# Kernel tuning notes

Measured on AMD Instinct MI355X. Metric: run time of the kernel, lower is better.

## Reference

```python
import jax, jax.numpy as jnp
import numpy as np

N, D, C, G, NNZ = 256, 1024, 50000, 4, 300000
EPS = 1e-5


def setup_inputs() -> dict:
    key = jax.random.key(0)
    ks = jax.random.split(key, 5)
    return {
        "output": jax.random.normal(ks[0], (N, D), jnp.float32),
        "wt2_w": jax.random.normal(ks[1], (C, D), jnp.float32) * 0.02,
        "wt2_b": jnp.zeros((C,), jnp.float32),
        "A_vals": jax.random.uniform(ks[2], (G, NNZ), dtype=jnp.float32),
        "vec": jnp.ones((G,), jnp.float32),
        "A_rows": jax.random.randint(ks[3], (G, NNZ), 0, C, jnp.int32),
        "A_cols": jax.random.randint(ks[4], (G, NNZ), 0, C, jnp.int32),
    }


def reference(output, wt2_w, wt2_b, A_vals, vec, A_rows, A_cols):
    # BatchNorm1d(embed_dim, affine=False), training-mode batch stats (biased var)
    mean = jnp.mean(output, axis=0)
    var = jnp.var(output, axis=0)
    h0 = (output - mean) * jax.lax.rsqrt(var + EPS)
    # wt2 linear + swish -> Z [N, C]
    h1 = h0 @ wt2_w.T + wt2_b
    Z = h1 * jax.nn.sigmoid(h1)
    # multi-graph sparse propagation: neighbors += spmm(A_i * vec[i], Z^T)^T
    # spmm out[b, r] = sum_{e: rows[e]==r} vals[e] * Z[b, cols[e]]
    Zt = Z.T  # [C, N]
    neighbors = jnp.zeros_like(Z)
    n_graphs = A_vals.shape[0]
    for i in range(n_graphs):  # small fixed number of relation graphs
        vals = A_vals[i] * vec[i]               # learnable per-graph weight
        msgs = Zt[A_cols[i]] * vals[:, None]    # [nnz, N] gathered messages
        agg = jax.ops.segment_sum(msgs, A_rows[i], num_segments=Zt.shape[0])  # [C, N]
        neighbors = neighbors + agg.T
    # residual combine
    return neighbors + Z
```

## Files before the change

kernel.cpp:

```cpp
#include <hip/hip_runtime.h>

typedef __attribute__((ext_vector_type(8))) short short8;
typedef __attribute__((ext_vector_type(4))) float floatx4;

#define C_DIM 50000
#define D_DIM 1024
#define N_DIM 256
#define G_NUM 4
#define NNZ_G 300000
#define E_TOT (G_NUM * NNZ_G)
#define SLOT_CAP 64

#define O_SB   0u
#define O_H0   8192u
#define O_ZT   532480u
#define O_CNT  26132480u
#define O_OFF  26332544u
#define O_CUR  26532608u
#define O_BS   26732672u
#define O_EDG  26733696u
#define O_CNT2 26132480u
#define O_SLOT 26332544u
#define SLOT_WS_NEEDED 51932544u

static __device__ __forceinline__ unsigned short f2bf(float f) {
    union { float f; unsigned u; } v; v.f = f;
    unsigned r = v.u + 0x7fffu + ((v.u >> 16) & 1u);
    return (unsigned short)(r >> 16);
}
static __device__ __forceinline__ float bf2f(unsigned short u) {
    union { unsigned u; float f; } v; v.u = ((unsigned)u) << 16;
    return v.f;
}

__global__ __launch_bounds__(256) void k_bnstats(const float* __restrict__ x,
                                                 float* __restrict__ scale,
                                                 float* __restrict__ bias) {
    __shared__ float sms[8][32], smss[8][32];
    const int t = threadIdx.x;
    const int dc = t & 31, grp = t >> 5;
    const int d = blockIdx.x * 32 + dc;
    float s = 0.f, ss = 0.f;
    for (int n = grp; n < N_DIM; n += 8) {
        float v = x[n * D_DIM + d];
        s += v; ss += v * v;
    }
    sms[grp][dc] = s; smss[grp][dc] = ss;
    __syncthreads();
    if (t < 32) {
        float S = 0.f, SS = 0.f;
#pragma unroll
        for (int g2 = 0; g2 < 8; ++g2) { S += sms[g2][t]; SS += smss[g2][t]; }
        float mean = S * (1.f / N_DIM);
        float var  = SS * (1.f / N_DIM) - mean * mean;
        float sc = rsqrtf(var + 1e-5f);
        int dd = blockIdx.x * 32 + t;
        scale[dd] = sc;
        bias[dd] = -mean * sc;
    }
}

__global__ __launch_bounds__(256) void k_h0f(const float* __restrict__ x,
                                             const float* __restrict__ scale,
                                             const float* __restrict__ bias,
                                             unsigned short* __restrict__ h0F) {
    int id = blockIdx.x * 256 + threadIdx.x;
    int b = id >> 7, kc = id & 127;
    const float4* xp = (const float4*)&x[(size_t)b * D_DIM + kc * 8];
    float4 f0 = xp[0], f1 = xp[1];
    const float4* sp = (const float4*)&scale[kc * 8];
    const float4* bp = (const float4*)&bias[kc * 8];
    float4 s0 = sp[0], s1 = sp[1], b0 = bp[0], b1 = bp[1];
    short8 o;
    o[0] = (short)f2bf(f0.x * s0.x + b0.x);
    o[1] = (short)f2bf(f0.y * s0.y + b0.y);
    o[2] = (short)f2bf(f0.z * s0.z + b0.z);
    o[3] = (short)f2bf(f0.w * s0.w + b0.w);
    o[4] = (short)f2bf(f1.x * s1.x + b1.x);
    o[5] = (short)f2bf(f1.y * s1.y + b1.y);
    o[6] = (short)f2bf(f1.z * s1.z + b1.z);
    o[7] = (short)f2bf(f1.w * s1.w + b1.w);
    int off = (b >> 4) * 16384 + (kc >> 2) * 512 + (kc & 3) * 128 + (b & 15) * 8;
    *(short8*)&h0F[off] = o;
}

__global__ __launch_bounds__(256) void k_gemm(const float* __restrict__ W,
                                              const float* __restrict__ wb,
                                              const unsigned short* __restrict__ h0F,
                                              unsigned short* __restrict__ Zt) {
    __shared__ unsigned short A_lds[2][8 * 64 * 8];
    const int t = threadIdx.x;
    const int w = t >> 6, lane = t & 63;
    const int m = lane & 15, g = lane >> 4;
    const int c0 = blockIdx.x * 64;

    const int srow = t >> 4;
    const int scc  = t & 15;
    const int s_kh = scc >> 3;
    const int s_g  = (scc >> 1) & 3;
    const int s_half = scc & 1;
    const int sbase = (srow + 16 * s_g) * 8 + s_half * 4;

    const unsigned short* hb = h0F + (size_t)(w * 4) * 16384 + lane * 8;

    float4 raA[4], raB[4];
    floatx4 acc[4][4];
#pragma unroll
    for (int i = 0; i < 4; ++i)
#pragma unroll
        for (int j = 0; j < 4; ++j) acc[i][j] = (floatx4)0.f;

#define LOADA(RA, ksv)                                                           \
    {                                                                            \
        const int kkv = (ksv) * 64;                                              \
        _Pragma("unroll")                                                        \
        for (int q = 0; q < 4; ++q) {                                            \
            int rr_ = c0 + q * 16 + srow; if (rr_ >= C_DIM) rr_ = C_DIM - 1;     \
            RA[q] = *(const float4*)&W[(size_t)rr_ * D_DIM + kkv + scc * 4];     \
        }                                                                        \
    }
#define STOREA(RA, bufv)                                                          \
    {                                                                             \
        _Pragma("unroll")                                                         \
        for (int q = 0; q < 4; ++q) {                                             \
            float4 f_ = RA[q];                                                    \
            unsigned p0_ = (unsigned)f2bf(f_.x) | ((unsigned)f2bf(f_.y) << 16);   \
            unsigned p1_ = (unsigned)f2bf(f_.z) | ((unsigned)f2bf(f_.w) << 16);   \
            *(uint2*)&A_lds[bufv][(s_kh * 4 + q) * 512 + sbase] =                 \
                make_uint2(p0_, p1_);                                             \
        }                                                                         \
    }
#define BARRIER()                                               \
    asm volatile("s_waitcnt lgkmcnt(0)" ::: "memory");          \
    __builtin_amdgcn_sched_barrier(0);                          \
    __builtin_amdgcn_s_barrier();                               \
    __builtin_amdgcn_sched_barrier(0);

#define GSTEP(ksv, RAs, RAl, CUR)                                                 \
    {                                                                             \
        short8 bfrag[2][4];                                                       \
        _Pragma("unroll")                                                         \
        for (int kh = 0; kh < 2; ++kh)                                            \
            _Pragma("unroll")                                                     \
            for (int j = 0; j < 4; ++j)                                           \
                bfrag[kh][j] = *(const short8*)&hb[(size_t)j * 16384 +            \
                                                  ((ksv) * 2 + kh) * 512];        \
        short8 afrag[2][4];                                                       \
        _Pragma("unroll")                                                         \
        for (int kh = 0; kh < 2; ++kh)                                            \
            _Pragma("unroll")                                                     \
            for (int i = 0; i < 4; ++i)                                           \
                afrag[kh][i] = *(const short8*)&A_lds[CUR][(kh * 4 + i) * 512 +   \
                                                          lane * 8];              \
        if ((ksv) < 15) STOREA(RAs, (CUR) ^ 1)                                    \
        if ((ksv) < 14) LOADA(RAl, (ksv) + 2)                                     \
        __builtin_amdgcn_s_setprio(1);                                            \
        _Pragma("unroll")                                                         \
        for (int kh = 0; kh < 2; ++kh)                                            \
            _Pragma("unroll")                                                     \
            for (int i = 0; i < 4; ++i)                                           \
                _Pragma("unroll")                                                 \
                for (int j = 0; j < 4; ++j)                                       \
                    acc[i][j] = __builtin_amdgcn_mfma_f32_16x16x32_bf16(          \
                        afrag[kh][i], bfrag[kh][j], acc[i][j], 0, 0, 0);          \
        __builtin_amdgcn_s_setprio(0);                                            \
        BARRIER()                                                                 \
    }

    LOADA(raA, 0)
    STOREA(raA, 0)
    LOADA(raB, 1)
    BARRIER()

#pragma unroll 1
    for (int ks2 = 0; ks2 < 16; ks2 += 2) {
        GSTEP(ks2,     raB, raA, 0)
        GSTEP(ks2 + 1, raA, raB, 1)
    }
#undef GSTEP
#undef LOADA
#undef STOREA
#undef BARRIER

#pragma unroll
    for (int i = 0; i < 4; ++i) {
#pragma unroll
        for (int j = 0; j < 4; ++j) {
            int b = w * 64 + j * 16 + m;
#pragma unroll
            for (int rr = 0; rr < 4; ++rr) {
                int c = c0 + i * 16 + g * 4 + rr;
                if (c < C_DIM) {
                    float x = acc[i][j][rr] + wb[c];
                    float z = x / (1.f + __expf(-x));
                    Zt[(size_t)c * 256 + b] = f2bf(z);
                }
            }
        }
    }
}

__global__ __launch_bounds__(256) void k_fscatter(const int* __restrict__ rows,
                                                  const int* __restrict__ cols,
                                                  const float* __restrict__ vals,
                                                  const float* __restrict__ vec,
                                                  int* __restrict__ cnt,
                                                  int2* __restrict__ slot) {
    int id = blockIdx.x * 256 + threadIdx.x;
    if (id < E_TOT) {
        int gidx = id / NNZ_G;
        float v = vals[id] * vec[gidx];
        int r = rows[id];
        int c = cols[id];
        int pos = atomicAdd(&cnt[r], 1);
        if (pos < SLOT_CAP) slot[r * SLOT_CAP + pos] = make_int2(c, __float_as_int(v));
    }
}

__global__ __launch_bounds__(256) void k_count(const int* __restrict__ rows,
                                               int* __restrict__ counts) {
    int id = blockIdx.x * 256 + threadIdx.x;
    if (id < E_TOT) atomicAdd(&counts[rows[id]], 1);
}

__global__ __launch_bounds__(256) void k_scan1(const int* __restrict__ counts,
                                               int* __restrict__ offsets,
                                               int* __restrict__ bsums) {
    __shared__ int sm[256];
    int t = threadIdx.x, i = blockIdx.x * 256 + t;
    int v = (i < C_DIM) ? counts[i] : 0;
    sm[t] = v; __syncthreads();
    for (int off = 1; off < 256; off <<= 1) {
        int x = (t >= off) ? sm[t - off] : 0;
        __syncthreads();
        sm[t] += x;
        __syncthreads();
    }
    if (i < C_DIM) offsets[i] = sm[t] - v;
    if (t == 255) bsums[blockIdx.x] = sm[255];
}

__global__ __launch_bounds__(256) void k_scan2(int* __restrict__ bsums,
                                               int* __restrict__ offsets) {
    __shared__ int sm[256];
    int t = threadIdx.x;
    int v = (t < 196) ? bsums[t] : 0;
    sm[t] = v; __syncthreads();
    for (int off = 1; off < 256; off <<= 1) {
        int x = (t >= off) ? sm[t - off] : 0;
        __syncthreads();
        sm[t] += x;
        __syncthreads();
    }
    if (t < 196) bsums[t] = sm[t] - v;
    if (t == 0) offsets[C_DIM] = sm[255];
}

__global__ __launch_bounds__(256) void k_scan3(const int* __restrict__ bsums,
                                               int* __restrict__ offsets,
                                               int* __restrict__ cursor) {
    int i = blockIdx.x * 256 + threadIdx.x;
    if (i < C_DIM) {
        int off = offsets[i] + bsums[blockIdx.x];
        offsets[i] = off;
        cursor[i] = off;
    }
}

__global__ __launch_bounds__(256) void k_scatter(const int* __restrict__ rows,
                                                 const int* __restrict__ cols,
                                                 const float* __restrict__ vals,
                                                 const float* __restrict__ vec,
                                                 int* __restrict__ cursor,
                                                 int2* __restrict__ edges) {
    int id = blockIdx.x * 256 + threadIdx.x;
    if (id < E_TOT) {
        int gidx = id / NNZ_G;
        float v = vals[id] * vec[gidx];
        int r = rows[id];
        int c = cols[id];
        int pos = atomicAdd(&cursor[r], 1);
        edges[pos] = make_int2(c, __float_as_int(v));
    }
}

static __device__ __forceinline__ void agg_row(const unsigned short* __restrict__ Zt,
                                               const int2* __restrict__ E,
                                               int s, int e, int base,
                                               float& a0, float& a1,
                                               float& a2, float& a3) {
    for (; s + 8 <= e; s += 8) {
        int2 e0 = E[s],     e1 = E[s + 1], e2 = E[s + 2], e3 = E[s + 3];
        int2 e4 = E[s + 4], e5 = E[s + 5], e6 = E[s + 6], e7 = E[s + 7];
        ushort4 g0 = *(const ushort4*)&Zt[(size_t)(unsigned)e0.x * 256 + base];
        ushort4 g1 = *(const ushort4*)&Zt[(size_t)(unsigned)e1.x * 256 + base];
        ushort4 g2 = *(const ushort4*)&Zt[(size_t)(unsigned)e2.x * 256 + base];
        ushort4 g3 = *(const ushort4*)&Zt[(size_t)(unsigned)e3.x * 256 + base];
        ushort4 g4 = *(const ushort4*)&Zt[(size_t)(unsigned)e4.x * 256 + base];
        ushort4 g5 = *(const ushort4*)&Zt[(size_t)(unsigned)e5.x * 256 + base];
        ushort4 g6 = *(const ushort4*)&Zt[(size_t)(unsigned)e6.x * 256 + base];
        ushort4 g7 = *(const ushort4*)&Zt[(size_t)(unsigned)e7.x * 256 + base];
        float v0 = __int_as_float(e0.y), v1 = __int_as_float(e1.y);
        float v2 = __int_as_float(e2.y), v3 = __int_as_float(e3.y);
        float v4 = __int_as_float(e4.y), v5 = __int_as_float(e5.y);
        float v6 = __int_as_float(e6.y), v7 = __int_as_float(e7.y);
        a0 += v0 * bf2f(g0.x) + v1 * bf2f(g1.x) + v2 * bf2f(g2.x) + v3 * bf2f(g3.x)
            + v4 * bf2f(g4.x) + v5 * bf2f(g5.x) + v6 * bf2f(g6.x) + v7 * bf2f(g7.x);
        a1 += v0 * bf2f(g0.y) + v1 * bf2f(g1.y) + v2 * bf2f(g2.y) + v3 * bf2f(g3.y)
            + v4 * bf2f(g4.y) + v5 * bf2f(g5.y) + v6 * bf2f(g6.y) + v7 * bf2f(g7.y);
        a2 += v0 * bf2f(g0.z) + v1 * bf2f(g1.z) + v2 * bf2f(g2.z) + v3 * bf2f(g3.z)
            + v4 * bf2f(g4.z) + v5 * bf2f(g5.z) + v6 * bf2f(g6.z) + v7 * bf2f(g7.z);
        a3 += v0 * bf2f(g0.w) + v1 * bf2f(g1.w) + v2 * bf2f(g2.w) + v3 * bf2f(g3.w)
            + v4 * bf2f(g4.w) + v5 * bf2f(g5.w) + v6 * bf2f(g6.w) + v7 * bf2f(g7.w);
    }
    for (; s < e; ++s) {
        int2 e0 = E[s];
        ushort4 g0 = *(const ushort4*)&Zt[(size_t)(unsigned)e0.x * 256 + base];
        float v0 = __int_as_float(e0.y);
        a0 += v0 * bf2f(g0.x);
        a1 += v0 * bf2f(g0.y);
        a2 += v0 * bf2f(g0.z);
        a3 += v0 * bf2f(g0.w);
    }
}

#define AGG_BODY(SBEG, SEND, EPTR)                                                \
    __shared__ float sm[32 * 256];                                                \
    const int t = threadIdx.x;                                                    \
    const int w = t >> 6, lane = t & 63;                                          \
    const int r0 = blockIdx.x * 32;                                               \
    const int base = lane * 4;                                                    \
    _Pragma("unroll 1")                                                           \
    for (int k = 0; k < 8; ++k) {                                                 \
        int lrow = w * 8 + k;                                                     \
        int r = __builtin_amdgcn_readfirstlane(r0 + lrow);                        \
        if (r < C_DIM) {                                                          \
            ushort4 z = *(const ushort4*)&Zt[(size_t)r * 256 + base];             \
            float a0 = bf2f(z.x), a1 = bf2f(z.y), a2 = bf2f(z.z), a3 = bf2f(z.w); \
            agg_row(Zt, (EPTR), (SBEG), (SEND), base, a0, a1, a2, a3);            \
            *(float4*)&sm[lrow * 256 + base] = make_float4(a0, a1, a2, a3);       \
        }                                                                         \
    }                                                                             \
    __syncthreads();                                                              \
    int rows_ = C_DIM - r0; if (rows_ > 32) rows_ = 32;                           \
    int nq = rows_ >> 2;                                                          \
    float4* op = (float4*)&out[(size_t)t * C_DIM + r0];                           \
    _Pragma("unroll 1")                                                           \
    for (int q = 0; q < nq; ++q) {                                                \
        float4 o;                                                                 \
        o.x = sm[(q * 4 + 0) * 256 + t];                                          \
        o.y = sm[(q * 4 + 1) * 256 + t];                                          \
        o.z = sm[(q * 4 + 2) * 256 + t];                                          \
        o.w = sm[(q * 4 + 3) * 256 + t];                                          \
        op[q] = o;                                                                \
    }

__global__ __launch_bounds__(256) void k_agg_csr(const unsigned short* __restrict__ Zt,
                                                 const int* __restrict__ offsets,
                                                 const int2* __restrict__ edges,
                                                 float* __restrict__ out) {
    AGG_BODY(offsets[r], offsets[r + 1], edges)
}

__global__ __launch_bounds__(256) void k_agg_slot(const unsigned short* __restrict__ Zt,
                                                  const int* __restrict__ cnt,
                                                  const int2* __restrict__ slot,
                                                  float* __restrict__ out) {
    AGG_BODY(r * SLOT_CAP, r * SLOT_CAP + min(cnt[r], SLOT_CAP), slot)
}
#undef AGG_BODY

extern "C" void kernel_launch(void* const* d_in, const int* in_sizes, int n_in,
                              void* d_out, int out_size, void* d_ws, size_t ws_size,
                              hipStream_t stream) {
    (void)in_sizes; (void)n_in; (void)out_size;
    const float* x     = (const float*)d_in[0];
    const float* W     = (const float*)d_in[1];
    const float* wb    = (const float*)d_in[2];
    const float* Avals = (const float*)d_in[3];
    const float* vec   = (const float*)d_in[4];
    const int*   Arows = (const int*)d_in[5];
    const int*   Acols = (const int*)d_in[6];
    float* out = (float*)d_out;
    char* ws = (char*)d_ws;

    float* scale = (float*)(ws + O_SB);
    float* bias  = scale + 1024;
    unsigned short* h0F = (unsigned short*)(ws + O_H0);
    unsigned short* Zt  = (unsigned short*)(ws + O_ZT);

    k_bnstats<<<32, 256, 0, stream>>>(x, scale, bias);
    k_h0f<<<128, 256, 0, stream>>>(x, scale, bias, h0F);

    if (ws_size >= (size_t)SLOT_WS_NEEDED) {
        int*  cnt  = (int*)(ws + O_CNT2);
        int2* slot = (int2*)(ws + O_SLOT);
        hipMemsetAsync(cnt, 0, C_DIM * sizeof(int), stream);
        k_fscatter<<<(E_TOT + 255) / 256, 256, 0, stream>>>(Arows, Acols, Avals, vec, cnt, slot);
        k_gemm<<<(C_DIM + 63) / 64, 256, 0, stream>>>(W, wb, h0F, Zt);
        k_agg_slot<<<(C_DIM + 31) / 32, 256, 0, stream>>>(Zt, cnt, slot, out);
    } else {
        int* counts  = (int*)(ws + O_CNT);
        int* offsets = (int*)(ws + O_OFF);
        int* cursor  = (int*)(ws + O_CUR);
        int* bsums   = (int*)(ws + O_BS);
        int2* edges  = (int2*)(ws + O_EDG);
        hipMemsetAsync(counts, 0, C_DIM * sizeof(int), stream);
        k_count<<<(E_TOT + 255) / 256, 256, 0, stream>>>(Arows, counts);
        k_gemm<<<(C_DIM + 63) / 64, 256, 0, stream>>>(W, wb, h0F, Zt);
        k_scan1<<<196, 256, 0, stream>>>(counts, offsets, bsums);
        k_scan2<<<1, 256, 0, stream>>>(bsums, offsets);
        k_scan3<<<196, 256, 0, stream>>>(bsums, offsets, cursor);
        k_scatter<<<(E_TOT + 255) / 256, 256, 0, stream>>>(Arows, Acols, Avals, vec, cursor, edges);
        k_agg_csr<<<(C_DIM + 31) / 32, 256, 0, stream>>>(Zt, offsets, edges, out);
    }
}
```

Baseline: 554.5 us.

## Prefetch GEMM B fragments, simplify A staging, and pad SpMM tail into unrolled loop

In the GEMM, the h0 B-fragments are now double-buffered in registers and loaded one k-step ahead, so their global load latency overlaps the MFMAs. The W tile staging is rearranged so each thread loads contiguous floats and writes whole short8 rows to LDS, replacing scattered uint2 stores. In the SpMM aggregation, the scalar tail loop is folded into the 8-wide loop by clamping indices and zeroing weights, which avoids serialized single-edge gathers. In exchange, register pressure rises and the padded iterations issue redundant gathers.

```diff
diff --git a/kernel.cpp b/kernel.cpp
--- a/kernel.cpp
+++ b/kernel.cpp
@@ -31,6 +31,15 @@
 static __device__ __forceinline__ float bf2f(unsigned short u) {
     union { unsigned u; float f; } v; v.u = ((unsigned)u) << 16;
     return v.f;
+}
+
+static __device__ __forceinline__ short8 cvt8(float4 a, float4 b) {
+    short8 r;
+    r[0] = (short)f2bf(a.x); r[1] = (short)f2bf(a.y);
+    r[2] = (short)f2bf(a.z); r[3] = (short)f2bf(a.w);
+    r[4] = (short)f2bf(b.x); r[5] = (short)f2bf(b.y);
+    r[6] = (short)f2bf(b.z); r[7] = (short)f2bf(b.w);
+    return r;
 }
 
 __global__ __launch_bounds__(256) void k_bnstats(const float* __restrict__ x,
@@ -88,47 +97,48 @@
                                               const float* __restrict__ wb,
                                               const unsigned short* __restrict__ h0F,
                                               unsigned short* __restrict__ Zt) {
-    __shared__ unsigned short A_lds[2][8 * 64 * 8];
+    __shared__ unsigned short A_lds[2][4096];
     const int t = threadIdx.x;
     const int w = t >> 6, lane = t & 63;
     const int m = lane & 15, g = lane >> 4;
     const int c0 = blockIdx.x * 64;
 
-    const int srow = t >> 4;
-    const int scc  = t & 15;
-    const int s_kh = scc >> 3;
-    const int s_g  = (scc >> 1) & 3;
-    const int s_half = scc & 1;
-    const int sbase = (srow + 16 * s_g) * 8 + s_half * 4;
+    int srow = c0 + w * 16 + m; if (srow >= C_DIM) srow = C_DIM - 1;
+    const float* pW = &W[(size_t)srow * D_DIM + g * 8];
+    const int sd0 = w * 512 + lane * 8;
+    const int sd1 = (w + 4) * 512 + lane * 8;
 
     const unsigned short* hb = h0F + (size_t)(w * 4) * 16384 + lane * 8;
 
     float4 raA[4], raB[4];
+    short8 bb[2][2][4];
     floatx4 acc[4][4];
 #pragma unroll
     for (int i = 0; i < 4; ++i)
 #pragma unroll
         for (int j = 0; j < 4; ++j) acc[i][j] = (floatx4)0.f;
 
-#define LOADA(RA, ksv)                                                           \
-    {                                                                            \
-        const int kkv = (ksv) * 64;                                              \
-        _Pragma("unroll")                                                        \
-        for (int q = 0; q < 4; ++q) {                                            \
-            int rr_ = c0 + q * 16 + srow; if (rr_ >= C_DIM) rr_ = C_DIM - 1;     \
-            RA[q] = *(const float4*)&W[(size_t)rr_ * D_DIM + kkv + scc * 4];     \
-        }                                                                        \
-    }
-#define STOREA(RA, bufv)                                                          \
-    {                                                                             \
-        _Pragma("unroll")                                                         \
-        for (int q = 0; q < 4; ++q) {                                             \
-            float4 f_ = RA[q];                                                    \
-            unsigned p0_ = (unsigned)f2bf(f_.x) | ((unsigned)f2bf(f_.y) << 16);   \
-            unsigned p1_ = (unsigned)f2bf(f_.z) | ((unsigned)f2bf(f_.w) << 16);   \
-            *(uint2*)&A_lds[bufv][(s_kh * 4 + q) * 512 + sbase] =                 \
-                make_uint2(p0_, p1_);                                             \
-        }                                                                         \
+#define LOADA(RA, ksv)                                          \
+    {                                                           \
+        const float* p_ = pW + (ksv) * 64;                      \
+        RA[0] = *(const float4*)(p_);                           \
+        RA[1] = *(const float4*)(p_ + 4);                       \
+        RA[2] = *(const float4*)(p_ + 32);                      \
+        RA[3] = *(const float4*)(p_ + 36);                      \
+    }
+#define STOREA(RA, bufv)                                        \
+    {                                                           \
+        *(short8*)&A_lds[bufv][sd0] = cvt8(RA[0], RA[1]);       \
+        *(short8*)&A_lds[bufv][sd1] = cvt8(RA[2], RA[3]);       \
+    }
+#define LOADB(S, ksv)                                                         \
+    {                                                                         \
+        _Pragma("unroll")                                                     \
+        for (int kh = 0; kh < 2; ++kh)                                        \
+            _Pragma("unroll")                                                 \
+            for (int j = 0; j < 4; ++j)                                       \
+                bb[S][kh][j] = *(const short8*)&hb[(size_t)j * 16384 +        \
+                                                  ((ksv) * 2 + kh) * 512];    \
     }
 #define BARRIER()                                               \
     asm volatile("s_waitcnt lgkmcnt(0)" ::: "memory");          \
@@ -136,22 +146,16 @@
     __builtin_amdgcn_s_barrier();                               \
     __builtin_amdgcn_sched_barrier(0);
 
-#define GSTEP(ksv, RAs, RAl, CUR)                                                 \
+#define GSTEP(ksv, RAs, RAl, CUR, BC, BN)                                         \
     {                                                                             \
-        short8 bfrag[2][4];                                                       \
-        _Pragma("unroll")                                                         \
-        for (int kh = 0; kh < 2; ++kh)                                            \
-            _Pragma("unroll")                                                     \
-            for (int j = 0; j < 4; ++j)                                           \
-                bfrag[kh][j] = *(const short8*)&hb[(size_t)j * 16384 +            \
-                                                  ((ksv) * 2 + kh) * 512];        \
-        short8 afrag[2][4];                                                       \
+        short8 af[2][4];                                                          \
         _Pragma("unroll")                                                         \
         for (int kh = 0; kh < 2; ++kh)                                            \
             _Pragma("unroll")                                                     \
             for (int i = 0; i < 4; ++i)                                           \
-                afrag[kh][i] = *(const short8*)&A_lds[CUR][(kh * 4 + i) * 512 +   \
-                                                          lane * 8];              \
+                af[kh][i] = *(const short8*)&A_lds[CUR][(kh * 4 + i) * 512 +      \
+                                                       lane * 8];                 \
+        if ((ksv) < 15) LOADB(BN, (ksv) + 1)                                      \
         if ((ksv) < 15) STOREA(RAs, (CUR) ^ 1)                                    \
         if ((ksv) < 14) LOADA(RAl, (ksv) + 2)                                     \
         __builtin_amdgcn_s_setprio(1);                                            \
@@ -162,7 +166,7 @@
                 _Pragma("unroll")                                                 \
                 for (int j = 0; j < 4; ++j)                                       \
                     acc[i][j] = __builtin_amdgcn_mfma_f32_16x16x32_bf16(          \
-                        afrag[kh][i], bfrag[kh][j], acc[i][j], 0, 0, 0);          \
+                        af[kh][i], bb[BC][kh][j], acc[i][j], 0, 0, 0);            \
         __builtin_amdgcn_s_setprio(0);                                            \
         BARRIER()                                                                 \
     }
@@ -170,16 +174,18 @@
     LOADA(raA, 0)
     STOREA(raA, 0)
     LOADA(raB, 1)
+    LOADB(0, 0)
     BARRIER()
 
 #pragma unroll 1
     for (int ks2 = 0; ks2 < 16; ks2 += 2) {
-        GSTEP(ks2,     raB, raA, 0)
-        GSTEP(ks2 + 1, raA, raB, 1)
+        GSTEP(ks2,     raB, raA, 0, 0, 1)
+        GSTEP(ks2 + 1, raA, raB, 1, 1, 0)
     }
 #undef GSTEP
 #undef LOADA
 #undef STOREA
+#undef LOADB
 #undef BARRIER
 
 #pragma unroll
@@ -289,9 +295,16 @@
                                                int s, int e, int base,
                                                float& a0, float& a1,
                                                float& a2, float& a3) {
-    for (; s + 8 <= e; s += 8) {
-        int2 e0 = E[s],     e1 = E[s + 1], e2 = E[s + 2], e3 = E[s + 3];
-        int2 e4 = E[s + 4], e5 = E[s + 5], e6 = E[s + 6], e7 = E[s + 7];
+#pragma unroll 1
+    for (; s < e; s += 8) {
+        int2 e0 = E[s];
+        int2 e1 = E[s + 1 < e ? s + 1 : e - 1];
+        int2 e2 = E[s + 2 < e ? s + 2 : e - 1];
+        int2 e3 = E[s + 3 < e ? s + 3 : e - 1];
+        int2 e4 = E[s + 4 < e ? s + 4 : e - 1];
+        int2 e5 = E[s + 5 < e ? s + 5 : e - 1];
+        int2 e6 = E[s + 6 < e ? s + 6 : e - 1];
+        int2 e7 = E[s + 7 < e ? s + 7 : e - 1];
         ushort4 g0 = *(const ushort4*)&Zt[(size_t)(unsigned)e0.x * 256 + base];
         ushort4 g1 = *(const ushort4*)&Zt[(size_t)(unsigned)e1.x * 256 + base];
         ushort4 g2 = *(const ushort4*)&Zt[(size_t)(unsigned)e2.x * 256 + base];
@@ -300,10 +313,14 @@
         ushort4 g5 = *(const ushort4*)&Zt[(size_t)(unsigned)e5.x * 256 + base];
         ushort4 g6 = *(const ushort4*)&Zt[(size_t)(unsigned)e6.x * 256 + base];
         ushort4 g7 = *(const ushort4*)&Zt[(size_t)(unsigned)e7.x * 256 + base];
-        float v0 = __int_as_float(e0.y), v1 = __int_as_float(e1.y);
-        float v2 = __int_as_float(e2.y), v3 = __int_as_float(e3.y);
-        float v4 = __int_as_float(e4.y), v5 = __int_as_float(e5.y);
-        float v6 = __int_as_float(e6.y), v7 = __int_as_float(e7.y);
+        float v0 = __int_as_float(e0.y);
+        float v1 = (s + 1 < e) ? __int_as_float(e1.y) : 0.f;
+        float v2 = (s + 2 < e) ? __int_as_float(e2.y) : 0.f;
+        float v3 = (s + 3 < e) ? __int_as_float(e3.y) : 0.f;
+        float v4 = (s + 4 < e) ? __int_as_float(e4.y) : 0.f;
+        float v5 = (s + 5 < e) ? __int_as_float(e5.y) : 0.f;
+        float v6 = (s + 6 < e) ? __int_as_float(e6.y) : 0.f;
+        float v7 = (s + 7 < e) ? __int_as_float(e7.y) : 0.f;
         a0 += v0 * bf2f(g0.x) + v1 * bf2f(g1.x) + v2 * bf2f(g2.x) + v3 * bf2f(g3.x)
             + v4 * bf2f(g4.x) + v5 * bf2f(g5.x) + v6 * bf2f(g6.x) + v7 * bf2f(g7.x);
         a1 += v0 * bf2f(g0.y) + v1 * bf2f(g1.y) + v2 * bf2f(g2.y) + v3 * bf2f(g3.y)
@@ -312,15 +329,6 @@
             + v4 * bf2f(g4.z) + v5 * bf2f(g5.z) + v6 * bf2f(g6.z) + v7 * bf2f(g7.z);
         a3 += v0 * bf2f(g0.w) + v1 * bf2f(g1.w) + v2 * bf2f(g2.w) + v3 * bf2f(g3.w)
             + v4 * bf2f(g4.w) + v5 * bf2f(g5.w) + v6 * bf2f(g6.w) + v7 * bf2f(g7.w);
-    }
-    for (; s < e; ++s) {
-        int2 e0 = E[s];
-        ushort4 g0 = *(const ushort4*)&Zt[(size_t)(unsigned)e0.x * 256 + base];
-        float v0 = __int_as_float(e0.y);
-        a0 += v0 * bf2f(g0.x);
-        a1 += v0 * bf2f(g0.y);
-        a2 += v0 * bf2f(g0.z);
-        a3 += v0 * bf2f(g0.w);
     }
 }
 
```

After: 559.8 us. About the same (+1.0%).
